# Optimization experiments

Hardware: AMD Instinct MI355X
Metric: run time of the kernel (lower is better)

The kernel has to match this reference:

```python
import jax, jax.numpy as jnp
import numpy as np

EPS = 1e-8

def dice(x, alpha, axis):
    # Dice activation: standardize over the batch axis, gate between x and alpha*x.
    mean = jnp.mean(x, axis=axis, keepdims=True)
    var = jnp.var(x, axis=axis, keepdims=True)
    p = jax.nn.sigmoid((x - mean) * jax.lax.rsqrt(var + EPS))
    return x * (p + alpha * (1.0 - p))

def setup_inputs() -> dict:
    key = jax.random.key(0)
    ks = jax.random.split(key, 12)
    B, L, D = 4096, 200, 64
    USER, ITEM, CATE = 100000, 100000, 1000
    AU_H = 36
    def dense(k, shape, fan_in):
        return jax.random.normal(k, shape, jnp.float32) * np.float32(1.0 / np.sqrt(fan_in))
    return {
        'user': jax.random.randint(ks[0], (B,), 0, USER),
        'hist': jax.random.randint(ks[1], (L, B), 0, ITEM),
        'item': jax.random.randint(ks[2], (B,), 0, ITEM),
        'cate': jax.random.randint(ks[3], (B,), 0, CATE),
        'u_emb': jax.random.normal(ks[4], (USER, D), jnp.float32) * 0.01,
        'i_emb': jax.random.normal(ks[5], (ITEM, D), jnp.float32) * 0.01,
        'c_emb': jax.random.normal(ks[6], (CATE, D), jnp.float32) * 0.01,
        'au_W1': dense(ks[7], (4 * D, AU_H), 4 * D), 'au_b1': jnp.zeros((AU_H,), jnp.float32),
        'au_alpha': jnp.zeros((AU_H,), jnp.float32),
        'au_W2': dense(ks[8], (AU_H, 1), AU_H), 'au_b2': jnp.zeros((1,), jnp.float32),
        'W1': dense(ks[9], (4 * D, 80), 4 * D), 'b1': jnp.zeros((80,), jnp.float32),
        'alpha1': jnp.zeros((80,), jnp.float32),
        'W2': dense(ks[10], (80, 40), 80), 'b2': jnp.zeros((40,), jnp.float32),
        'alpha2': jnp.zeros((40,), jnp.float32),
        'W3': dense(ks[11], (40, 2), 40), 'b3': jnp.zeros((2,), jnp.float32),
    }

def reference(user, hist, item, cate, u_emb, i_emb, c_emb,
              au_W1, au_b1, au_alpha, au_W2, au_b2,
              W1, b1, alpha1, W2, b2, alpha2, W3, b3):
    u = u_emb[user]            # [B, D]
    it = i_emb[item]           # [B, D]
    c = c_emb[cate]            # [B, D]
    h = i_emb[hist]            # [L, B, D] history item embeddings
    itb = jnp.broadcast_to(it[None], h.shape)
    # Activation unit over all history steps at once (vectorizes the per-step loop)
    feat = jnp.concatenate([h, itb, h - itb, h * itb], axis=-1)  # [L, B, 4D]
    a = dice(feat @ au_W1 + au_b1, au_alpha, axis=1)             # batch stats per step
    w = a @ au_W2 + au_b2                                        # [L, B, 1]
    # Weighted-sum pooling; original detaches history embeddings in the sum
    cur = jnp.sum(w * jax.lax.stop_gradient(h), axis=0)          # [B, D]
    z = jnp.concatenate([u, it, c, cur], axis=-1)                # [B, 4D]
    z = dice(z @ W1 + b1, alpha1, axis=0)
    z = dice(z @ W2 + b2, alpha2, axis=0)
    return z @ W3 + b3                                           # [B, 2]
```

## Files before the change

### kernel.cpp

```cpp
#include <hip/hip_runtime.h>
#include <hip/hip_bf16.h>

#define B_ 4096
#define L_ 200
#define D_ 64
#define NJ 36
#define H1 80
#define H2 40
#define NROW (B_*L_)
#define TPW 2
#define BROWS (4*16*TPW)
#define NGRID2 (NROW/BROWS)
#define BCH 128
#define BPC (B_/BCH)
#define LJ (L_*NJ)
#define NITEM 100000
#define EPS_ 1e-8f

typedef short bf16x8 __attribute__((ext_vector_type(8)));
typedef float f32x4 __attribute__((ext_vector_type(4)));
typedef unsigned short u16x8 __attribute__((ext_vector_type(8)));
typedef unsigned short u16x4 __attribute__((ext_vector_type(4)));

__device__ __forceinline__ float sigmoidf_(float x) { return 1.0f / (1.0f + __expf(-x)); }

__device__ __forceinline__ unsigned short bfr(float x) {
    unsigned u = __float_as_uint(x);
    return (unsigned short)((u + 0x7fffu + ((u >> 16) & 1u)) >> 16);
}
__device__ __forceinline__ float bf2f(unsigned short v) {
    return __uint_as_float(((unsigned)v) << 16);
}
__device__ __forceinline__ unsigned cvtpk(float lo, float hi) {
    unsigned r;
    asm("v_cvt_pk_bf16_f32 %0, %1, %2" : "=v"(r) : "v"(lo), "v"(hi));
    return r;
}
__device__ __forceinline__ u16x8 pk8u(float4 a, float4 b) {
    union { unsigned u[4]; u16x8 v; } r;
    r.u[0] = cvtpk(a.x, a.y); r.u[1] = cvtpk(a.z, a.w);
    r.u[2] = cvtpk(b.x, b.y); r.u[3] = cvtpk(b.z, b.w);
    return r.v;
}
__device__ __forceinline__ bf16x8 asbf(u16x8 v) {
    union { u16x8 u; bf16x8 b; } c; c.u = v; return c.b;
}
__device__ __forceinline__ bf16x8 bsub8(u16x8 a, u16x8 b) {
    union { unsigned u[4]; bf16x8 v; } r;
    #pragma unroll
    for (int i = 0; i < 4; ++i)
        r.u[i] = cvtpk(bf2f(a[2*i]) - bf2f(b[2*i]), bf2f(a[2*i+1]) - bf2f(b[2*i+1]));
    return r.v;
}
__device__ __forceinline__ bf16x8 bmul8(u16x8 a, u16x8 b) {
    union { unsigned u[4]; bf16x8 v; } r;
    #pragma unroll
    for (int i = 0; i < 4; ++i)
        r.u[i] = cvtpk(bf2f(a[2*i]) * bf2f(b[2*i]), bf2f(a[2*i+1]) * bf2f(b[2*i+1]));
    return r.v;
}

__global__ __launch_bounds__(256) void k_cvt(const float* __restrict__ src, unsigned short* __restrict__ dst) {
    int g = blockIdx.x * 256 + threadIdx.x;
    if (g >= NITEM * D_ / 8) return;
    const float4* s4 = (const float4*)src;
    float4 a = s4[g * 2], b = s4[g * 2 + 1];
    ((u16x8*)dst)[g] = pk8u(a, b);
}

__global__ __launch_bounds__(256) void k_tr(const int* __restrict__ hist, int* __restrict__ histT) {
    __shared__ int tile[32][33];
    int b0 = blockIdx.x * 32, l0 = blockIdx.y * 32;
    int tx = threadIdx.x & 31, ty = threadIdx.x >> 5;
    #pragma unroll
    for (int i = 0; i < 4; ++i) {
        int l = l0 + ty + i * 8;
        if (l < L_) tile[ty + i * 8][tx] = hist[l * B_ + b0 + tx];
    }
    __syncthreads();
    #pragma unroll
    for (int i = 0; i < 4; ++i) {
        int b = b0 + ty + i * 8;
        int l = l0 + tx;
        if (l < L_) histT[b * L_ + l] = tile[tx][ty + i * 8];
    }
}

__global__ void k_prep(const float* __restrict__ auW1, unsigned short* __restrict__ wfrag) {
    int s = blockIdx.x * 256 + threadIdx.x;
    if (s >= 24 * 64 * 8) return;
    int e = s & 7, lane = (s >> 3) & 63, ks = (s >> 9) & 7, nt = s >> 12;
    int n = nt * 16 + (lane & 15);
    int k = ks * 32 + ((lane >> 4) << 3) + e;
    wfrag[s] = (n < NJ) ? bfr(auW1[k * NJ + n]) : (unsigned short)0;
}

__global__ void k_coef(const float* __restrict__ alpha, const float* __restrict__ auW2,
                       float* __restrict__ c01) {
    int j = threadIdx.x;
    if (j < NJ) {
        float a = alpha[j], w = auW2[j];
        c01[2 * j] = w * a;
        c01[2 * j + 1] = w * (1.f - a);
    }
}

__global__ __launch_bounds__(256, 4) void k_gemm(const int* __restrict__ histT,
        const int* __restrict__ item, const unsigned short* __restrict__ i_emb16,
        const unsigned short* __restrict__ wfrag, const float* __restrict__ aub1,
        unsigned short* __restrict__ A16) {
    __shared__ __align__(16) unsigned short wls[24 * 64 * 8];
    int tid = threadIdx.x;
    int wv = tid >> 6, lane = tid & 63;
    int m = lane & 15, kg = lane >> 4;

    int wt0 = (blockIdx.x * 4 + wv) * TPW;
    int g0 = wt0 * 16 + m;
    int g1 = g0 + 16;
    int b0 = g0 / L_, l0 = g0 - b0 * L_;
    int b1 = g1 / L_, l1 = g1 - b1 * L_;
    int h0 = histT[b0 * L_ + l0];
    int i0 = item[b0];
    int h1 = histT[b1 * L_ + l1];
    int i1 = item[b1];

    {
        const float4* src = (const float4*)wfrag;
        float4* dst = (float4*)wls;
        #pragma unroll
        for (int i = 0; i < 6; ++i) dst[i * 256 + tid] = src[i * 256 + tid];
    }

    const u16x8* hp0 = (const u16x8*)(i_emb16 + (long)h0 * D_);
    const u16x8* ip0 = (const u16x8*)(i_emb16 + (long)i0 * D_);
    const u16x8* hp1 = (const u16x8*)(i_emb16 + (long)h1 * D_);
    const u16x8* ip1 = (const u16x8*)(i_emb16 + (long)i1 * D_);
    u16x8 ha = hp0[kg], hb = hp0[4 + kg];
    u16x8 ta = ip0[kg], tb = ip0[4 + kg];
    u16x8 ea = hp1[kg], eb = hp1[4 + kg];
    u16x8 ua = ip1[kg], ub = ip1[4 + kg];

    bf16x8 af0[8], af1[8];
    af0[0] = asbf(ha); af0[1] = asbf(hb);
    af0[2] = asbf(ta); af0[3] = asbf(tb);
    af0[4] = bsub8(ha, ta); af0[5] = bsub8(hb, tb);
    af0[6] = bmul8(ha, ta); af0[7] = bmul8(hb, tb);
    af1[0] = asbf(ea); af1[1] = asbf(eb);
    af1[2] = asbf(ua); af1[3] = asbf(ub);
    af1[4] = bsub8(ea, ua); af1[5] = bsub8(eb, ub);
    af1[6] = bmul8(ea, ua); af1[7] = bmul8(eb, ub);

    __syncthreads();

    const bf16x8* wf = (const bf16x8*)wls;
    f32x4 c00 = {0.f,0.f,0.f,0.f}, c01 = c00, c02 = c00;
    f32x4 c10 = c00, c11 = c00, c12 = c00;
    #pragma unroll
    for (int ks = 0; ks < 8; ++ks) {
        bf16x8 w0 = wf[ks * 64 + lane];
        bf16x8 w1 = wf[(8 + ks) * 64 + lane];
        bf16x8 w2 = wf[(16 + ks) * 64 + lane];
        c00 = __builtin_amdgcn_mfma_f32_16x16x32_bf16(af0[ks], w0, c00, 0, 0, 0);
        c10 = __builtin_amdgcn_mfma_f32_16x16x32_bf16(af1[ks], w0, c10, 0, 0, 0);
        c01 = __builtin_amdgcn_mfma_f32_16x16x32_bf16(af0[ks], w1, c01, 0, 0, 0);
        c11 = __builtin_amdgcn_mfma_f32_16x16x32_bf16(af1[ks], w1, c11, 0, 0, 0);
        c02 = __builtin_amdgcn_mfma_f32_16x16x32_bf16(af0[ks], w2, c02, 0, 0, 0);
        c12 = __builtin_amdgcn_mfma_f32_16x16x32_bf16(af1[ks], w2, c12, 0, 0, 0);
    }

    float bias0 = aub1[m], bias1 = aub1[16 + m];
    float bias2 = (m < 4) ? aub1[32 + m] : 0.f;
    long rb0 = (long)wt0 * 16 + kg * 4;
    #pragma unroll
    for (int i = 0; i < 4; ++i) {
        unsigned short* o = A16 + (rb0 + i) * NJ;
        o[m]      = bfr(c00[i] + bias0);
        o[16 + m] = bfr(c01[i] + bias1);
        if (m < 4) o[32 + m] = bfr(c02[i] + bias2);
    }
    long rb1 = rb0 + 16;
    #pragma unroll
    for (int i = 0; i < 4; ++i) {
        unsigned short* o = A16 + (rb1 + i) * NJ;
        o[m]      = bfr(c10[i] + bias0);
        o[16 + m] = bfr(c11[i] + bias1);
        if (m < 4) o[32 + m] = bfr(c12[i] + bias2);
    }
}

__global__ __launch_bounds__(256) void k_stats_p(const unsigned short* __restrict__ A16,
        float* __restrict__ sp, float* __restrict__ sq) {
    int t = blockIdx.x * 256 + threadIdx.x;
    if (t >= LJ / 8) return;
    int c = blockIdx.y;
    const u16x8* base = (const u16x8*)(A16 + (long)c * BPC * LJ) + t;
    float s[8], q[8];
    #pragma unroll
    for (int i = 0; i < 8; ++i) { s[i] = 0.f; q[i] = 0.f; }
    #pragma unroll 4
    for (int b = 0; b < BPC; ++b) {
        u16x8 v = base[(long)b * (LJ / 8)];
        #pragma unroll
        for (int i = 0; i < 8; ++i) {
            float f = bf2f(v[i]);
            s[i] += f; q[i] += f * f;
        }
    }
    #pragma unroll
    for (int i = 0; i < 8; ++i) {
        sp[(long)c * LJ + t * 8 + i] = s[i];
        sq[(long)c * LJ + t * 8 + i] = q[i];
    }
}

__global__ void k_stats_fin(const float* __restrict__ sp, const float* __restrict__ sq,
                            unsigned* __restrict__ mr16) {
    int lj = blockIdx.x * 256 + threadIdx.x;
    if (lj >= LJ) return;
    float s = 0.f, q = 0.f;
    for (int c = 0; c < BCH; ++c) { s += sp[(long)c * LJ + lj]; q += sq[(long)c * LJ + lj]; }
    float m = s * (1.0f / B_);
    float v = fmaxf(q * (1.0f / B_) - m * m, 0.f);
    mr16[lj] = cvtpk(m, rsqrtf(v + EPS_));
}

__global__ __launch_bounds__(256) void k_w(const unsigned short* __restrict__ A16,
        const unsigned* __restrict__ mr16, const float* __restrict__ c01,
        const float* __restrict__ aub2, float* __restrict__ wbuf) {
    __shared__ __align__(16) unsigned short aL[256 * NJ];
    int tid = threadIdx.x;
    const u16x8* gsrc = (const u16x8*)(A16 + (long)blockIdx.x * 256 * NJ);
    u16x8* ld = (u16x8*)aL;
    #pragma unroll
    for (int i = 0; i < 4; ++i) ld[i * 256 + tid] = gsrc[i * 256 + tid];
    if (tid < 128) ld[1024 + tid] = gsrc[1024 + tid];
    __syncthreads();

    int row = blockIdx.x * 256 + tid;
    int l = row % L_;
    const u16x4* Ab4 = (const u16x4*)(aL + tid * NJ);
    const u16x8* mrp = (const u16x8*)(mr16 + l * NJ);
    float w = aub2[0];
    #pragma unroll
    for (int cgi = 0; cgi < 9; ++cgi) {
        u16x4 av = Ab4[cgi];
        u16x8 mr = mrp[cgi];
        #pragma unroll
        for (int i = 0; i < 4; ++i) {
            int j = cgi * 4 + i;
            float s = bf2f(av[i]);
            float p = sigmoidf_((s - bf2f(mr[2 * i])) * bf2f(mr[2 * i + 1]));
            w += s * fmaf(c01[2 * j + 1], p, c01[2 * j]);
        }
    }
    wbuf[row] = w;
}

__global__ __launch_bounds__(256) void k_pool(const int* __restrict__ histT,
        const int* __restrict__ user, const int* __restrict__ item, const int* __restrict__ cate,
        const float* __restrict__ u_emb, const float* __restrict__ i_emb, const float* __restrict__ c_emb,
        const unsigned short* __restrict__ i_emb16, const float* __restrict__ wbuf,
        float* __restrict__ z_buf) {
    __shared__ float part[4][D_];
    int b = blockIdx.x;
    int tid = threadIdx.x;
    int q = tid >> 6, d = tid & 63;
    const int* rp = histT + b * L_;
    const float* wp = wbuf + (long)b * L_;
    float s = 0.f;
    int l0 = q * 50;
    #pragma unroll 5
    for (int i = 0; i < 50; ++i) {
        int ll = l0 + i;
        s += wp[ll] * bf2f(i_emb16[(long)rp[ll] * D_ + d]);
    }
    part[q][d] = s;
    __syncthreads();
    if (q == 0) {
        z_buf[b * 256 + 192 + d] = part[0][d] + part[1][d] + part[2][d] + part[3][d];
    } else if (q == 1) {
        z_buf[b * 256 + d]       = u_emb[(long)user[b] * D_ + d];
    } else if (q == 2) {
        z_buf[b * 256 + 64 + d]  = i_emb[(long)item[b] * D_ + d];
    } else {
        z_buf[b * 256 + 128 + d] = c_emb[(long)cate[b] * D_ + d];
    }
}

__global__ __launch_bounds__(256) void k_mlp1(const float* __restrict__ z_buf,
        const float* __restrict__ W1, const float* __restrict__ b1,
        float* __restrict__ y1, float* __restrict__ gs1, float* __restrict__ gq1) {
    __shared__ float zt[16 * 256];
    __shared__ float w_s[256 * H1];
    __shared__ float ls[H1], lq[H1];
    int tid = threadIdx.x;
    int b0 = blockIdx.x * 16;
    for (int i = tid; i < 16 * 256; i += 256) zt[i] = z_buf[b0 * 256 + i];
    for (int i = tid; i < 256 * H1; i += 256) w_s[i] = W1[i];
    if (tid < H1) { ls[tid] = 0.f; lq[tid] = 0.f; }
    __syncthreads();
    for (int o = tid; o < 16 * H1; o += 256) {
        int bl = o / H1, j = o - bl * H1;
        float s = b1[j];
        for (int k = 0; k < 256; ++k) s += zt[bl * 256 + k] * w_s[k * H1 + j];
        y1[(b0 + bl) * H1 + j] = s;
        atomicAdd(&ls[j], s); atomicAdd(&lq[j], s * s);
    }
    __syncthreads();
    if (tid < H1) { atomicAdd(&gs1[tid], ls[tid]); atomicAdd(&gq1[tid], lq[tid]); }
}

__global__ void k_fin(const float* __restrict__ gs, const float* __restrict__ gq,
                      float* __restrict__ m, float* __restrict__ r, int n) {
    int i = blockIdx.x * blockDim.x + threadIdx.x;
    if (i < n) {
        float mm = gs[i] * (1.0f / B_);
        float v = fmaxf(gq[i] * (1.0f / B_) - mm * mm, 0.f);
        m[i] = mm; r[i] = rsqrtf(v + EPS_);
    }
}

__global__ __launch_bounds__(256) void k_mlp2(const float* __restrict__ y1,
        const float* __restrict__ m1, const float* __restrict__ r1, const float* __restrict__ alpha1,
        const float* __restrict__ W2, const float* __restrict__ b2,
        float* __restrict__ y2, float* __restrict__ gs2, float* __restrict__ gq2) {
    __shared__ float at[16 * H1];
    __shared__ float w_s[H1 * H2];
    __shared__ float ls[H2], lq[H2];
    int tid = threadIdx.x;
    int b0 = blockIdx.x * 16;
    for (int i = tid; i < 16 * H1; i += 256) {
        float x = y1[b0 * H1 + i];
        int j = i % H1;
        float p = sigmoidf_((x - m1[j]) * r1[j]);
        at[i] = x * (p + alpha1[j] * (1.f - p));
    }
    for (int i = tid; i < H1 * H2; i += 256) w_s[i] = W2[i];
    if (tid < H2) { ls[tid] = 0.f; lq[tid] = 0.f; }
    __syncthreads();
    for (int o = tid; o < 16 * H2; o += 256) {
        int bl = o / H2, j = o - bl * H2;
        float s = b2[j];
        #pragma unroll
        for (int k = 0; k < H1; ++k) s += at[bl * H1 + k] * w_s[k * H2 + j];
        y2[(b0 + bl) * H2 + j] = s;
        atomicAdd(&ls[j], s); atomicAdd(&lq[j], s * s);
    }
    __syncthreads();
    if (tid < H2) { atomicAdd(&gs2[tid], ls[tid]); atomicAdd(&gq2[tid], lq[tid]); }
}

__global__ void k_out(const float* __restrict__ y2,
        const float* __restrict__ m2, const float* __restrict__ r2, const float* __restrict__ alpha2,
        const float* __restrict__ W3, const float* __restrict__ b3, float* __restrict__ out) {
    int b = blockIdx.x * blockDim.x + threadIdx.x;
    if (b >= B_) return;
    float s0 = b3[0], s1 = b3[1];
    #pragma unroll
    for (int k = 0; k < H2; ++k) {
        float x = y2[b * H2 + k];
        float p = sigmoidf_((x - m2[k]) * r2[k]);
        float a = x * (p + alpha2[k] * (1.f - p));
        s0 += a * W3[k * 2];
        s1 += a * W3[k * 2 + 1];
    }
    out[b * 2] = s0;
    out[b * 2 + 1] = s1;
}

extern "C" void kernel_launch(void* const* d_in, const int* in_sizes, int n_in,
                              void* d_out, int out_size, void* d_ws, size_t ws_size,
                              hipStream_t stream) {
    const int*   user  = (const int*)d_in[0];
    const int*   hist  = (const int*)d_in[1];
    const int*   item  = (const int*)d_in[2];
    const int*   cate  = (const int*)d_in[3];
    const float* u_emb = (const float*)d_in[4];
    const float* i_emb = (const float*)d_in[5];
    const float* c_emb = (const float*)d_in[6];
    const float* auW1  = (const float*)d_in[7];
    const float* aub1  = (const float*)d_in[8];
    const float* aual  = (const float*)d_in[9];
    const float* auW2  = (const float*)d_in[10];
    const float* aub2  = (const float*)d_in[11];
    const float* W1    = (const float*)d_in[12];
    const float* b1    = (const float*)d_in[13];
    const float* al1   = (const float*)d_in[14];
    const float* W2    = (const float*)d_in[15];
    const float* b2    = (const float*)d_in[16];
    const float* al2   = (const float*)d_in[17];
    const float* W3    = (const float*)d_in[18];
    const float* b3    = (const float*)d_in[19];

    unsigned short* A16    = (unsigned short*)d_ws;
    unsigned short* wfrag  = A16 + (size_t)NROW * NJ;
    unsigned short* iemb16 = wfrag + 24 * 64 * 8;
    float* ws = (float*)(iemb16 + (size_t)NITEM * D_);
    size_t off = 0;
    float* sp    = ws + off; off += (size_t)BCH * LJ;
    float* sq    = ws + off; off += (size_t)BCH * LJ;
    unsigned* mr16 = (unsigned*)(ws + off); off += LJ;
    float* c01   = ws + off; off += 2 * NJ;
    float* gs1   = ws + off; off += H1;
    float* gq1   = ws + off; off += H1;
    float* gs2   = ws + off; off += H2;
    float* gq2   = ws + off; off += H2;
    float* m1    = ws + off; off += H1;
    float* r1    = ws + off; off += H1;
    float* m2    = ws + off; off += H2;
    float* r2    = ws + off; off += H2;
    float* z_buf = ws + off; off += (size_t)B_ * 256;
    float* y1    = ws + off; off += (size_t)B_ * H1;
    float* y2    = ws + off; off += (size_t)B_ * H2;
    float* wbuf  = ws + off; off += NROW;
    int* histT   = (int*)(ws + off); off += NROW;

    hipMemsetAsync(gs1, 0, (2 * H1 + 2 * H2) * sizeof(float), stream);

    k_cvt<<<(NITEM * D_ / 8 + 255) / 256, 256, 0, stream>>>(i_emb, iemb16);
    {
        dim3 g(B_ / 32, (L_ + 31) / 32);
        k_tr<<<g, 256, 0, stream>>>(hist, histT);
    }
    k_prep<<<48, 256, 0, stream>>>(auW1, wfrag);
    k_coef<<<1, 64, 0, stream>>>(aual, auW2, c01);
    k_gemm<<<NGRID2, 256, 0, stream>>>(histT, item, iemb16, wfrag, aub1, A16);
    {
        dim3 g(4, BCH);
        k_stats_p<<<g, 256, 0, stream>>>(A16, sp, sq);
    }
    k_stats_fin<<<(LJ + 255) / 256, 256, 0, stream>>>(sp, sq, mr16);
    k_w<<<NROW / 256, 256, 0, stream>>>(A16, mr16, c01, aub2, wbuf);
    k_pool<<<B_, 256, 0, stream>>>(histT, user, item, cate, u_emb, i_emb, c_emb,
                                   iemb16, wbuf, z_buf);
    k_mlp1<<<B_ / 16, 256, 0, stream>>>(z_buf, W1, b1, y1, gs1, gq1);
    k_fin<<<1, 128, 0, stream>>>(gs1, gq1, m1, r1, H1);
    k_mlp2<<<B_ / 16, 256, 0, stream>>>(y1, m1, r1, al1, W2, b2, y2, gs2, gq2);
    k_fin<<<1, 64, 0, stream>>>(gs2, gq2, m2, r2, H2);
    k_out<<<B_ / 256, 256, 0, stream>>>(y2, m2, r2, al2, W3, b3, (float*)d_out);
}
```

Baseline: 186.1 us.

## Fuse preprocessing kernels into one launch and compact third weight tile

Merges the embedding conversion, history transpose, weight fragment prep, coefficient computation and the accumulator memset into a single multi-role kernel, removing four launches and a memset. It also packs the third N-tile of the attention weight fragments so that only the 4 valid columns are stored, which shrinks the shared-memory weight buffer and the global-to-LDS copy. Lanes that fall outside those columns read a zeroed pad. The occupancy hint on the GEMM rises from 4 to 6 blocks per CU, which may squeeze registers.

```diff
diff --git a/kernel.cpp b/kernel.cpp
--- a/kernel.cpp
+++ b/kernel.cpp
@@ -17,6 +17,14 @@
 #define NITEM 100000
 #define EPS_ 1e-8f
 
+#define NCVT 3125
+#define NTRX 128
+#define NTRY 7
+#define NTR (NTRX*NTRY)
+#define WF_SZ 9216
+#define NPREP (WF_SZ/256)
+#define NPRE (NCVT+NTR+NPREP+1)
+
 typedef short bf16x8 __attribute__((ext_vector_type(8)));
 typedef float f32x4 __attribute__((ext_vector_type(4)));
 typedef unsigned short u16x8 __attribute__((ext_vector_type(8)));
@@ -60,56 +68,63 @@
     return r.v;
 }
 
-__global__ __launch_bounds__(256) void k_cvt(const float* __restrict__ src, unsigned short* __restrict__ dst) {
-    int g = blockIdx.x * 256 + threadIdx.x;
-    if (g >= NITEM * D_ / 8) return;
-    const float4* s4 = (const float4*)src;
-    float4 a = s4[g * 2], b = s4[g * 2 + 1];
-    ((u16x8*)dst)[g] = pk8u(a, b);
-}
-
-__global__ __launch_bounds__(256) void k_tr(const int* __restrict__ hist, int* __restrict__ histT) {
+__global__ __launch_bounds__(256) void k_pre(const float* __restrict__ i_emb,
+        unsigned short* __restrict__ iemb16, const int* __restrict__ hist,
+        int* __restrict__ histT, const float* __restrict__ auW1,
+        unsigned short* __restrict__ wfrag, const float* __restrict__ alpha,
+        const float* __restrict__ auW2, float* __restrict__ c01, float* __restrict__ gzero) {
     __shared__ int tile[32][33];
-    int b0 = blockIdx.x * 32, l0 = blockIdx.y * 32;
-    int tx = threadIdx.x & 31, ty = threadIdx.x >> 5;
-    #pragma unroll
-    for (int i = 0; i < 4; ++i) {
-        int l = l0 + ty + i * 8;
-        if (l < L_) tile[ty + i * 8][tx] = hist[l * B_ + b0 + tx];
-    }
-    __syncthreads();
-    #pragma unroll
-    for (int i = 0; i < 4; ++i) {
-        int b = b0 + ty + i * 8;
-        int l = l0 + tx;
-        if (l < L_) histT[b * L_ + l] = tile[tx][ty + i * 8];
-    }
-}
-
-__global__ void k_prep(const float* __restrict__ auW1, unsigned short* __restrict__ wfrag) {
-    int s = blockIdx.x * 256 + threadIdx.x;
-    if (s >= 24 * 64 * 8) return;
-    int e = s & 7, lane = (s >> 3) & 63, ks = (s >> 9) & 7, nt = s >> 12;
-    int n = nt * 16 + (lane & 15);
-    int k = ks * 32 + ((lane >> 4) << 3) + e;
-    wfrag[s] = (n < NJ) ? bfr(auW1[k * NJ + n]) : (unsigned short)0;
-}
-
-__global__ void k_coef(const float* __restrict__ alpha, const float* __restrict__ auW2,
-                       float* __restrict__ c01) {
-    int j = threadIdx.x;
-    if (j < NJ) {
-        float a = alpha[j], w = auW2[j];
-        c01[2 * j] = w * a;
-        c01[2 * j + 1] = w * (1.f - a);
-    }
-}
-
-__global__ __launch_bounds__(256, 4) void k_gemm(const int* __restrict__ histT,
+    int bid = blockIdx.x, tid = threadIdx.x;
+    if (bid < NCVT) {
+        int g = bid * 256 + tid;
+        const float4* s4 = (const float4*)i_emb;
+        float4 a = s4[g * 2], b = s4[g * 2 + 1];
+        ((u16x8*)iemb16)[g] = pk8u(a, b);
+    } else if (bid < NCVT + NTR) {
+        int t = bid - NCVT;
+        int b0 = (t % NTRX) * 32, l0 = (t / NTRX) * 32;
+        int tx = tid & 31, ty = tid >> 5;
+        #pragma unroll
+        for (int i = 0; i < 4; ++i) {
+            int l = l0 + ty + i * 8;
+            if (l < L_) tile[ty + i * 8][tx] = hist[l * B_ + b0 + tx];
+        }
+        __syncthreads();
+        #pragma unroll
+        for (int i = 0; i < 4; ++i) {
+            int b = b0 + ty + i * 8;
+            int l = l0 + tx;
+            if (l < L_) histT[b * L_ + l] = tile[tx][ty + i * 8];
+        }
+    } else if (bid < NCVT + NTR + NPREP) {
+        int s = (bid - (NCVT + NTR)) * 256 + tid;
+        int k, n;
+        if (s < 8192) {
+            int e = s & 7, lane = (s >> 3) & 63, ks = (s >> 9) & 7, nt = s >> 12;
+            n = nt * 16 + (lane & 15);
+            k = ks * 32 + ((lane >> 4) << 3) + e;
+        } else {
+            int t2 = s - 8192;
+            int e = t2 & 7, slot = (t2 >> 3) & 15, ks = t2 >> 7;
+            n = 32 + (slot & 3);
+            k = ks * 32 + (slot >> 2) * 8 + e;
+        }
+        wfrag[s] = bfr(auW1[k * NJ + n]);
+    } else {
+        if (tid < NJ) {
+            float a = alpha[tid], w = auW2[tid];
+            c01[2 * tid] = w * a;
+            c01[2 * tid + 1] = w * (1.f - a);
+        }
+        if (tid < 2 * H1 + 2 * H2) gzero[tid] = 0.f;
+    }
+}
+
+__global__ __launch_bounds__(256, 6) void k_gemm(const int* __restrict__ histT,
         const int* __restrict__ item, const unsigned short* __restrict__ i_emb16,
         const unsigned short* __restrict__ wfrag, const float* __restrict__ aub1,
         unsigned short* __restrict__ A16) {
-    __shared__ __align__(16) unsigned short wls[24 * 64 * 8];
+    __shared__ __align__(16) unsigned short wls[WF_SZ + 16];
     int tid = threadIdx.x;
     int wv = tid >> 6, lane = tid & 63;
     int m = lane & 15, kg = lane >> 4;
@@ -128,7 +143,10 @@
         const float4* src = (const float4*)wfrag;
         float4* dst = (float4*)wls;
         #pragma unroll
-        for (int i = 0; i < 6; ++i) dst[i * 256 + tid] = src[i * 256 + tid];
+        for (int i = 0; i < 4; ++i) dst[i * 256 + tid] = src[i * 256 + tid];
+        if (tid < 128) dst[1024 + tid] = src[1024 + tid];
+        if (tid == 128) *(float4*)(wls + WF_SZ) = make_float4(0.f, 0.f, 0.f, 0.f);
+        if (tid == 129) *(float4*)(wls + WF_SZ + 8) = make_float4(0.f, 0.f, 0.f, 0.f);
     }
 
     const u16x8* hp0 = (const u16x8*)(i_emb16 + (long)h0 * D_);
@@ -153,30 +171,33 @@
     __syncthreads();
 
     const bf16x8* wf = (const bf16x8*)wls;
-    f32x4 c00 = {0.f,0.f,0.f,0.f}, c01 = c00, c02 = c00;
+    bool v2 = (m < 4);
+    int base2 = (kg * 4 + m) * 8;
+    f32x4 c00 = {0.f,0.f,0.f,0.f}, c01v = c00, c02 = c00;
     f32x4 c10 = c00, c11 = c00, c12 = c00;
     #pragma unroll
     for (int ks = 0; ks < 8; ++ks) {
         bf16x8 w0 = wf[ks * 64 + lane];
         bf16x8 w1 = wf[(8 + ks) * 64 + lane];
-        bf16x8 w2 = wf[(16 + ks) * 64 + lane];
+        int o2 = v2 ? (8192 + ks * 128 + base2) : WF_SZ;
+        bf16x8 w2 = *(const bf16x8*)(wls + o2);
         c00 = __builtin_amdgcn_mfma_f32_16x16x32_bf16(af0[ks], w0, c00, 0, 0, 0);
         c10 = __builtin_amdgcn_mfma_f32_16x16x32_bf16(af1[ks], w0, c10, 0, 0, 0);
-        c01 = __builtin_amdgcn_mfma_f32_16x16x32_bf16(af0[ks], w1, c01, 0, 0, 0);
+        c01v = __builtin_amdgcn_mfma_f32_16x16x32_bf16(af0[ks], w1, c01v, 0, 0, 0);
         c11 = __builtin_amdgcn_mfma_f32_16x16x32_bf16(af1[ks], w1, c11, 0, 0, 0);
         c02 = __builtin_amdgcn_mfma_f32_16x16x32_bf16(af0[ks], w2, c02, 0, 0, 0);
         c12 = __builtin_amdgcn_mfma_f32_16x16x32_bf16(af1[ks], w2, c12, 0, 0, 0);
     }
 
     float bias0 = aub1[m], bias1 = aub1[16 + m];
-    float bias2 = (m < 4) ? aub1[32 + m] : 0.f;
+    float bias2 = v2 ? aub1[32 + m] : 0.f;
     long rb0 = (long)wt0 * 16 + kg * 4;
     #pragma unroll
     for (int i = 0; i < 4; ++i) {
         unsigned short* o = A16 + (rb0 + i) * NJ;
         o[m]      = bfr(c00[i] + bias0);
-        o[16 + m] = bfr(c01[i] + bias1);
-        if (m < 4) o[32 + m] = bfr(c02[i] + bias2);
+        o[16 + m] = bfr(c01v[i] + bias1);
+        if (v2) o[32 + m] = bfr(c02[i] + bias2);
     }
     long rb1 = rb0 + 16;
     #pragma unroll
@@ -184,7 +205,7 @@
         unsigned short* o = A16 + (rb1 + i) * NJ;
         o[m]      = bfr(c10[i] + bias0);
         o[16 + m] = bfr(c11[i] + bias1);
-        if (m < 4) o[32 + m] = bfr(c12[i] + bias2);
+        if (v2) o[32 + m] = bfr(c12[i] + bias2);
     }
 }
 
@@ -394,7 +415,7 @@
 
     unsigned short* A16    = (unsigned short*)d_ws;
     unsigned short* wfrag  = A16 + (size_t)NROW * NJ;
-    unsigned short* iemb16 = wfrag + 24 * 64 * 8;
+    unsigned short* iemb16 = wfrag + WF_SZ;
     float* ws = (float*)(iemb16 + (size_t)NITEM * D_);
     size_t off = 0;
     float* sp    = ws + off; off += (size_t)BCH * LJ;
@@ -415,15 +436,8 @@
     float* wbuf  = ws + off; off += NROW;
     int* histT   = (int*)(ws + off); off += NROW;
 
-    hipMemsetAsync(gs1, 0, (2 * H1 + 2 * H2) * sizeof(float), stream);
-
-    k_cvt<<<(NITEM * D_ / 8 + 255) / 256, 256, 0, stream>>>(i_emb, iemb16);
-    {
-        dim3 g(B_ / 32, (L_ + 31) / 32);
-        k_tr<<<g, 256, 0, stream>>>(hist, histT);
-    }
-    k_prep<<<48, 256, 0, stream>>>(auW1, wfrag);
-    k_coef<<<1, 64, 0, stream>>>(aual, auW2, c01);
+    k_pre<<<NPRE, 256, 0, stream>>>(i_emb, iemb16, hist, histT, auW1, wfrag,
+                                    aual, auW2, c01, gs1);
     k_gemm<<<NGRID2, 256, 0, stream>>>(histT, item, iemb16, wfrag, aub1, A16);
     {
         dim3 g(4, BCH);
```

Measured after the change: 205.6 us. 1.11x slower.
